# Kernel optimization log

Hardware: AMD Instinct MI355X
Metric: run time of the kernel (lower is better)

## Reference

```python
import jax, jax.numpy as jnp
import numpy as np

H = 128          # hidden_dim
B = 4096         # number of graphs (segments)
N = 1048576      # total nodes
NUM_OBS = 1


def setup_inputs() -> dict:
    key = jax.random.key(0)
    ks = jax.random.split(key, 10)
    h = jax.random.normal(ks[0], (N, H), dtype=jnp.float32)
    batch = jnp.sort(jax.random.randint(ks[1], (N,), 0, B, dtype=jnp.int64))
    s = 1.0 / np.sqrt(H)
    s2 = 1.0 / np.sqrt(2 * H)
    # gate: Linear(H,H) -> tanh -> Linear(H,1)
    gate_w1 = jax.random.uniform(ks[2], (H, H), jnp.float32, -s, s)
    gate_b1 = jax.random.uniform(ks[3], (H,), jnp.float32, -s, s)
    gate_w2 = jax.random.uniform(ks[4], (H, 1), jnp.float32, -s, s)
    gate_b2 = jax.random.uniform(ks[5], (1,), jnp.float32, -s, s)
    # mlp: Linear(2H,H) -> ReLU -> Linear(H,num_obs)  (dropout off in eval)
    mlp_w1 = jax.random.uniform(ks[6], (2 * H, H), jnp.float32, -s2, s2)
    mlp_b1 = jax.random.uniform(ks[7], (H,), jnp.float32, -s2, s2)
    mlp_w2 = jax.random.uniform(ks[8], (H, NUM_OBS), jnp.float32, -s, s)
    mlp_b2 = jax.random.uniform(ks[9], (NUM_OBS,), jnp.float32, -s, s)
    return {"h": h, "batch": batch,
            "gate_w1": gate_w1, "gate_b1": gate_b1,
            "gate_w2": gate_w2, "gate_b2": gate_b2,
            "mlp_w1": mlp_w1, "mlp_b1": mlp_b1,
            "mlp_w2": mlp_w2, "mlp_b2": mlp_b2}


def reference(h, batch, gate_w1, gate_b1, gate_w2, gate_b2,
              mlp_w1, mlp_b1, mlp_w2, mlp_b2):
    # gate scores per node: (N,)
    score = (jnp.tanh(h @ gate_w1 + gate_b1) @ gate_w2 + gate_b2)[:, 0]
    # segment softmax over nodes of each graph (numerically stable)
    seg_max = jax.ops.segment_max(score, batch, num_segments=B)
    e = jnp.exp(score - seg_max[batch])
    seg_sum = jax.ops.segment_sum(e, batch, num_segments=B)
    attn = e / seg_sum[batch]                      # (N,)
    # attention-weighted sum pooling: (B, H)
    g_attn = jax.ops.segment_sum(h * attn[:, None], batch, num_segments=B)
    # max pooling: (B, H)
    g_max = jax.ops.segment_max(h, batch, num_segments=B)
    g = jnp.concatenate([g_attn, g_max], axis=-1)  # (B, 2H)
    hidden = jax.nn.relu(g @ mlp_w1 + mlp_b1)
    return hidden @ mlp_w2 + mlp_b2               # (B, NUM_OBS)
```

## Files before the change

### kernel.cpp

```cpp
#include <hip/hip_runtime.h>
#include <hip/hip_bf16.h>
#include <cfloat>

#define HD 128

typedef float f32x4 __attribute__((ext_vector_type(4)));
typedef __bf16 bf16x8 __attribute__((ext_vector_type(8)));

__global__ void seg_bounds_kernel(const int* __restrict__ batch, int n, int nseg,
                                  int* __restrict__ seg_start) {
  int b = blockIdx.x * blockDim.x + threadIdx.x;
  if (b > nseg) return;
  if (b == nseg) { seg_start[b] = n; return; }
  int lo = 0, hi = n;
  while (lo < hi) {
    int mid = (lo + hi) >> 1;
    if (batch[mid] < b) lo = mid + 1; else hi = mid;
  }
  seg_start[b] = lo;
}


#define LOAD_TILE(BUF, T)                                                   \
  {                                                                         \
    const int nIt_ = (T) * 16 + lr;                                         \
    const size_t row_ = (size_t)s0 + (size_t)min(nIt_, lenm1);              \
    const float* hp_ = h + row_ * HD + 8 * kl;                              \
    _Pragma("unroll")                                                       \
    for (int kt = 0; kt < 4; ++kt) {                                        \
      *reinterpret_cast<float4*>(&BUF[8 * kt]) =                            \
          *reinterpret_cast<const float4*>(hp_ + 32 * kt);                  \
      *reinterpret_cast<float4*>(&BUF[8 * kt + 4]) =                        \
          *reinterpret_cast<const float4*>(hp_ + 32 * kt + 4);              \
    }                                                                       \
  }

#define PROC_TILE(BUF, T)                                                   \
  {                                                                         \
    const bool valid_ = ((T) * 16 + lr) < len;                              \
    bf16x8 a_[4];                                                           \
    _Pragma("unroll")                                                       \
    for (int kt = 0; kt < 4; ++kt)                                          \
      _Pragma("unroll")                                                     \
      for (int j = 0; j < 8; ++j) a_[kt][j] = (__bf16)BUF[8 * kt + j];      \
                 \
    asm volatile("" : "+v"(Cb));                                            \
    f32x4 macc_[8];                                                         \
    _Pragma("unroll")                                                       \
    for (int f = 0; f < 8; ++f) macc_[f] = (f32x4){0.f, 0.f, 0.f, 0.f};     \
    _Pragma("unroll")                                                       \
    for (int kt = 0; kt < 4; ++kt) {                                        \
      const char* bp_ = reinterpret_cast<const char*>(sWt) +                \
                        (Cb + ((kt ^ hi2) << 6));                           \
      bf16x8 bfr_[8];                                                       \
      _Pragma("unroll")                                                     \
      for (int f = 0; f < 8; ++f)                                           \
        bfr_[f] = *reinterpret_cast<const bf16x8*>(bp_ + f * 4096);         \
      _Pragma("unroll")                                                     \
      for (int f = 0; f < 8; ++f)                                           \
        macc_[f] =                                                          \
            __builtin_amdgcn_mfma_f32_16x16x32_bf16(a_[kt], bfr_[f],        \
                                                    macc_[f], 0, 0, 0);     \
    }                                                                       \
    float p2_[4] = {0.f, 0.f, 0.f, 0.f};                                    \
    _Pragma("unroll")                                                       \
    for (int f = 0; f < 8; ++f) {                                           \
      _Pragma("unroll")                                                     \
      for (int r = 0; r < 4; ++r) {                                         \
        const float xe_ = fmaf(LOG2E2, macc_[f][r], b1s[f]);                \
        const float e_ = exp2f(xe_);                                        \
        const float t_ = __builtin_amdgcn_rcpf(1.f + e_);                   \
        p2_[r] = fmaf(t_, w2r[f], p2_[r]);                                  \
      }                                                                     \
    }                                                                       \
    _Pragma("unroll")                                                       \
    for (int r = 0; r < 4; ++r) {                                           \
      p2_[r] += __shfl_xor(p2_[r], 1, 16);                                  \
      p2_[r] += __shfl_xor(p2_[r], 2, 16);                                  \
      p2_[r] += __shfl_xor(p2_[r], 4, 16);                                  \
      p2_[r] += __shfl_xor(p2_[r], 8, 16);                                  \
    }                                                                       \
    const int rr_ = lr & 3;                                                 \
    const float psel_ =                                                     \
        rr_ == 0 ? p2_[0] : (rr_ == 1 ? p2_[1] : (rr_ == 2 ? p2_[2]         \
                                                            : p2_[3]));     \
    const float sc_ = __shfl(psel_, ((lr >> 2) << 4) | (lr & 3), 64);       \
    const float w_ = valid_ ? exp2f(sc_ * NEG2LOG2E) : 0.f;                 \
    s += w_;                                                                \
    _Pragma("unroll")                                                       \
    for (int j = 0; j < 32; ++j) {                                          \
      acc[j] = fmaf(BUF[j], w_, acc[j]);                                    \
      gm[j] = fmaxf(gm[j], BUF[j]);                                         \
    }                                                                       \
  }

__global__ __launch_bounds__(256, 2) void fused_pool_kernel(
    const float* __restrict__ h, const float* __restrict__ w1,
    const float* __restrict__ b1, const float* __restrict__ w2,
    const int* __restrict__ seg_start, float* __restrict__ g, int B)
{
  __shared__ __bf16 sWt[HD * HD];

  for (int i = threadIdx.x; i < HD * HD / 4; i += 256) {
    const int k = i >> 5;
    const int c4 = (i & 31) << 2;
    const float4 v = reinterpret_cast<const float4*>(w1)[i];
    const float vv[4] = {v.x, v.y, v.z, v.w};
#pragma unroll
    for (int q = 0; q < 4; ++q) {
      const int c = c4 + q;
      sWt[c * HD + ((((k >> 3) ^ (c & 15)) << 3) | (k & 7))] = (__bf16)vv[q];
    }
  }
  __syncthreads();

  const float LOG2E2    = 2.88539008177792681f;
  const float NEG2LOG2E = -2.88539008177792681f;

  const int lane = threadIdx.x & 63;
  const int wid  = threadIdx.x >> 6;
  const int lr   = lane & 15;
  const int kl   = lane >> 4;

  float w2r[8], b1s[8];
#pragma unroll
  for (int f = 0; f < 8; ++f) {
    w2r[f] = w2[16 * f + lr];
    b1s[f] = LOG2E2 * b1[16 * f + lr];
  }

  const int hi2 = (lr >> 2) & 3;
  int Cb = lr * 256 + ((kl ^ (lr & 3)) << 4);

  const int segStride = gridDim.x * 4;
  for (int b = blockIdx.x * 4 + wid; b < B; b += segStride) {
    const int s0  = seg_start[b];
    const int len = seg_start[b + 1] - s0;
    const int lenm1 = len - 1;
    const int nt  = (len + 15) >> 4;

    float s = 0.f;
    float acc[32], gm[32];
#pragma unroll
    for (int j = 0; j < 32; ++j) { acc[j] = 0.f; gm[j] = -FLT_MAX; }

    if (nt > 0) {
      float hA[32], hB[32];
      LOAD_TILE(hA, 0)
      int t = 0;
      for (; t + 1 < nt; t += 2) {
        LOAD_TILE(hB, t + 1)
        PROC_TILE(hA, t)
        if (t + 2 < nt) LOAD_TILE(hA, t + 2)
        PROC_TILE(hB, t + 1)
      }
      if (t < nt) PROC_TILE(hA, t)
    }

#pragma unroll
    for (int off = 1; off <= 8; off <<= 1) {
      s += __shfl_xor(s, off, 16);
#pragma unroll
      for (int j = 0; j < 32; ++j) {
        acc[j] += __shfl_xor(acc[j], off, 16);
        gm[j] = fmaxf(gm[j], __shfl_xor(gm[j], off, 16));
      }
    }

    if (lr == 0) {
      const float invS = (s > 0.f) ? 1.f / s : 0.f;
#pragma unroll
      for (int kt = 0; kt < 4; ++kt) {
        const int fb = 32 * kt + 8 * kl;
        float4 va, vb, ma, mb;
        va.x = acc[8*kt+0]*invS; va.y = acc[8*kt+1]*invS;
        va.z = acc[8*kt+2]*invS; va.w = acc[8*kt+3]*invS;
        vb.x = acc[8*kt+4]*invS; vb.y = acc[8*kt+5]*invS;
        vb.z = acc[8*kt+6]*invS; vb.w = acc[8*kt+7]*invS;
        ma.x = gm[8*kt+0]; ma.y = gm[8*kt+1]; ma.z = gm[8*kt+2]; ma.w = gm[8*kt+3];
        mb.x = gm[8*kt+4]; mb.y = gm[8*kt+5]; mb.z = gm[8*kt+6]; mb.w = gm[8*kt+7];
        *reinterpret_cast<float4*>(&g[(size_t)b * 256 + fb])           = va;
        *reinterpret_cast<float4*>(&g[(size_t)b * 256 + fb + 4])       = vb;
        *reinterpret_cast<float4*>(&g[(size_t)b * 256 + 128 + fb])     = ma;
        *reinterpret_cast<float4*>(&g[(size_t)b * 256 + 128 + fb + 4]) = mb;
      }
    }
  }
}

__global__ __launch_bounds__(512) void mlp_kernel(
    const float* __restrict__ g, const float* __restrict__ w1,
    const float* __restrict__ b1, const float* __restrict__ w2,
    const float* __restrict__ b2, float* __restrict__ out)
{
  __shared__ float sg[4][256];
  __shared__ float sred[4][2];
  const int t = threadIdx.x;
  const int sidx = t >> 7;
  const int u = t & 127;
  const int b0 = blockIdx.x * 4;
  sg[sidx][u]       = g[(size_t)(b0 + sidx) * 256 + u];
  sg[sidx][u + 128] = g[(size_t)(b0 + sidx) * 256 + 128 + u];
  __syncthreads();
  float acc = b1[u];
#pragma unroll 8
  for (int k = 0; k < 256; ++k)
    acc = fmaf(sg[sidx][k], w1[k * HD + u], acc);
  float v = fmaxf(acc, 0.f) * w2[u];
#pragma unroll
  for (int off = 32; off >= 1; off >>= 1) v += __shfl_xor(v, off, 64);
  if ((t & 63) == 0) sred[sidx][(t >> 6) & 1] = v;
  __syncthreads();
  if (u == 0) out[b0 + sidx] = sred[sidx][0] + sred[sidx][1] + b2[0];
}

extern "C" void kernel_launch(void* const* d_in, const int* in_sizes, int n_in,
                              void* d_out, int out_size, void* d_ws, size_t ws_size,
                              hipStream_t stream) {
  const float* h       = (const float*)d_in[0];
  const int*   batch   = (const int*)d_in[1];
  const float* gate_w1 = (const float*)d_in[2];
  const float* gate_b1 = (const float*)d_in[3];
  const float* gate_w2 = (const float*)d_in[4];
  const float* mlp_w1  = (const float*)d_in[6];
  const float* mlp_b1  = (const float*)d_in[7];
  const float* mlp_w2  = (const float*)d_in[8];
  const float* mlp_b2  = (const float*)d_in[9];
  float* out = (float*)d_out;

  const int N = in_sizes[0] / HD;
  const int B = out_size;

  char* ws = (char*)d_ws;
  float* g   = (float*)ws;
  int*   seg = (int*)(ws + (size_t)B * 256 * 4);

  seg_bounds_kernel<<<(B + 256) / 256, 256, 0, stream>>>(batch, N, B, seg);
  fused_pool_kernel<<<1024, 256, 0, stream>>>(h, gate_w1, gate_b1, gate_w2,
                                              seg, g, B);
  mlp_kernel<<<B / 4, 512, 0, stream>>>(g, mlp_w1, mlp_b1, mlp_w2, mlp_b2, out);
}
```

Baseline: 185.4 us.

## Triple-buffer node tiles, split MFMA accumulators, and use DPP row reductions

The per-segment loop moves from double to triple buffering of 16-row h tiles, so two tiles are in flight while one is processed. Tail handling is dropped: loads are clamped to the last row and extra processed tiles are masked by a validity check. The gate MFMA is split into two halves of four accumulators to lower peak register use. The 16-lane score reduction uses DPP row_ror instead of shuffles. Each segment may now process up to two redundant tiles, and the third buffer adds register pressure.

```diff
diff --git a/kernel.cpp b/kernel.cpp
--- a/kernel.cpp
+++ b/kernel.cpp
@@ -20,6 +20,12 @@
   seg_start[b] = lo;
 }
 
+template <int CTRL>
+__device__ __forceinline__ float dpp_ror(float v) {
+  return __int_as_float(__builtin_amdgcn_update_dpp(
+      0, __float_as_int(v), CTRL, 0xF, 0xF, true));
+}
+
 
 #define LOAD_TILE(BUF, T)                                                   \
   {                                                                         \
@@ -45,40 +51,44 @@
       for (int j = 0; j < 8; ++j) a_[kt][j] = (__bf16)BUF[8 * kt + j];      \
                  \
     asm volatile("" : "+v"(Cb));                                            \
-    f32x4 macc_[8];                                                         \
-    _Pragma("unroll")                                                       \
-    for (int f = 0; f < 8; ++f) macc_[f] = (f32x4){0.f, 0.f, 0.f, 0.f};     \
-    _Pragma("unroll")                                                       \
-    for (int kt = 0; kt < 4; ++kt) {                                        \
-      const char* bp_ = reinterpret_cast<const char*>(sWt) +                \
-                        (Cb + ((kt ^ hi2) << 6));                           \
-      bf16x8 bfr_[8];                                                       \
-      _Pragma("unroll")                                                     \
-      for (int f = 0; f < 8; ++f)                                           \
-        bfr_[f] = *reinterpret_cast<const bf16x8*>(bp_ + f * 4096);         \
-      _Pragma("unroll")                                                     \
-      for (int f = 0; f < 8; ++f)                                           \
-        macc_[f] =                                                          \
-            __builtin_amdgcn_mfma_f32_16x16x32_bf16(a_[kt], bfr_[f],        \
-                                                    macc_[f], 0, 0, 0);     \
-    }                                                                       \
     float p2_[4] = {0.f, 0.f, 0.f, 0.f};                                    \
     _Pragma("unroll")                                                       \
-    for (int f = 0; f < 8; ++f) {                                           \
-      _Pragma("unroll")                                                     \
-      for (int r = 0; r < 4; ++r) {                                         \
-        const float xe_ = fmaf(LOG2E2, macc_[f][r], b1s[f]);                \
-        const float e_ = exp2f(xe_);                                        \
-        const float t_ = __builtin_amdgcn_rcpf(1.f + e_);                   \
-        p2_[r] = fmaf(t_, w2r[f], p2_[r]);                                  \
+    for (int hf = 0; hf < 2; ++hf) {                                        \
+      f32x4 macc_[4];                                                       \
+      _Pragma("unroll")                                                     \
+      for (int fh = 0; fh < 4; ++fh) macc_[fh] = (f32x4){0.f, 0.f, 0.f, 0.f}; \
+      _Pragma("unroll")                                                     \
+      for (int kt = 0; kt < 4; ++kt) {                                      \
+        const char* bp_ = reinterpret_cast<const char*>(sWt) +              \
+                          (Cb + ((kt ^ hi2) << 6)) + hf * 16384;            \
+        bf16x8 bfr_[4];                                                     \
+        _Pragma("unroll")                                                   \
+        for (int fh = 0; fh < 4; ++fh)                                      \
+          bfr_[fh] = *reinterpret_cast<const bf16x8*>(bp_ + fh * 4096);     \
+        _Pragma("unroll")                                                   \
+        for (int fh = 0; fh < 4; ++fh)                                      \
+          macc_[fh] = __builtin_amdgcn_mfma_f32_16x16x32_bf16(              \
+              a_[kt], bfr_[fh], macc_[fh], 0, 0, 0);                        \
       }                                                                     \
-    }                                                                       \
+      _Pragma("unroll")                                                     \
+      for (int fh = 0; fh < 4; ++fh) {                                      \
+        const int f_ = 4 * hf + fh;                                         \
+        _Pragma("unroll")                                                   \
+        for (int r = 0; r < 4; ++r) {                                       \
+          const float xe_ = fmaf(LOG2E2, macc_[fh][r], b1s[f_]);            \
+          const float e_ = exp2f(xe_);                                      \
+          const float t_ = __builtin_amdgcn_rcpf(1.f + e_);                 \
+          p2_[r] = fmaf(t_, w2r[f_], p2_[r]);                               \
+        }                                                                   \
+      }                                                                     \
+    }                                                                       \
+       \
     _Pragma("unroll")                                                       \
     for (int r = 0; r < 4; ++r) {                                           \
-      p2_[r] += __shfl_xor(p2_[r], 1, 16);                                  \
-      p2_[r] += __shfl_xor(p2_[r], 2, 16);                                  \
-      p2_[r] += __shfl_xor(p2_[r], 4, 16);                                  \
-      p2_[r] += __shfl_xor(p2_[r], 8, 16);                                  \
+      p2_[r] += dpp_ror<0x121>(p2_[r]);                                     \
+      p2_[r] += dpp_ror<0x122>(p2_[r]);                                     \
+      p2_[r] += dpp_ror<0x124>(p2_[r]);                                     \
+      p2_[r] += dpp_ror<0x128>(p2_[r]);                                     \
     }                                                                       \
     const int rr_ = lr & 3;                                                 \
     const float psel_ =                                                     \
@@ -145,16 +155,17 @@
     for (int j = 0; j < 32; ++j) { acc[j] = 0.f; gm[j] = -FLT_MAX; }
 
     if (nt > 0) {
-      float hA[32], hB[32];
+      float hA[32], hB[32], hC[32];
       LOAD_TILE(hA, 0)
-      int t = 0;
-      for (; t + 1 < nt; t += 2) {
-        LOAD_TILE(hB, t + 1)
+      LOAD_TILE(hB, 1)
+      for (int t = 0; t < nt; t += 3) {
+        LOAD_TILE(hC, t + 2)
         PROC_TILE(hA, t)
-        if (t + 2 < nt) LOAD_TILE(hA, t + 2)
+        LOAD_TILE(hA, t + 3)
         PROC_TILE(hB, t + 1)
+        LOAD_TILE(hB, t + 4)
+        PROC_TILE(hC, t + 2)
       }
-      if (t < nt) PROC_TILE(hA, t)
     }
 
 #pragma unroll
```

Measured after the change: 273.7 us. 1.48x slower.
